# Kernel optimization log

Hardware: AMD Instinct MI355X
Metric: run time of the kernel (lower is better)

The kernel has to match this reference:

```python
import jax, jax.numpy as jnp
import numpy as np

OBS_LEN = 8
B = 262144
H = 16   # lstm hidden / MADE hidden / cond dim
D = 2    # trajectory input dim / flow dim
N_FLOWS = 4
CLAMP = 5.0


def _masks():
    # MADE masks for num_inputs=2, num_hidden=16 (ikostrikov get_mask)
    in_deg = jnp.arange(D) % D                      # [0, 1]
    hid_deg = jnp.zeros((H,), jnp.float32)          # arange(16) % (2-1) == 0
    out_deg = (jnp.arange(2 * D) % D - 1).astype(jnp.float32)  # [-1,0,-1,0]
    input_mask = (hid_deg[:, None] >= in_deg[None, :].astype(jnp.float32)).astype(jnp.float32)  # [16,2]
    hidden_mask = jnp.ones((H, H), jnp.float32)     # all degrees 0 -> full
    output_mask = (out_deg[:, None] >= hid_deg[None, :]).astype(jnp.float32)  # [4,16]
    return input_mask, hidden_mask, output_mask


def _made_ma(x, cond, p, masks):
    # x: [B,2], cond: [B,16] -> m, a: [B,2]
    im, hm, om = masks
    jW, jb, cW, hW, hb, oW, ob = p
    h = x @ (jW * im).T + jb + cond @ cW.T      # joiner (masked) + cond linear (no bias)
    h = jax.nn.relu(h)
    h = jax.nn.relu(h @ (hW * hm).T + hb)       # trunk hidden masked linear
    out = h @ (oW * om).T + ob                  # trunk output masked linear -> [B,4]
    m, a = out[:, :D], out[:, D:]
    a = CLAMP * jnp.tanh(a / CLAMP)             # soft log-scale clamp (clamp_flow)
    return m, a


def _made_inverse(u, cond, p, masks):
    x = jnp.zeros_like(u)
    for i in range(D):
        m, a = _made_ma(x, cond, p, masks)
        x = x.at[:, i].set(u[:, i] * jnp.exp(a[:, i]) + m[:, i])
    return x


def _maf_sample(noise, cond, made_params, masks):
    # modules = [MADE0,Rev,MADE1,Rev,MADE2,Rev,MADE3,Rev]; sample runs inverse in reversed order
    x = noise
    for k in reversed(range(N_FLOWS)):
        x = x[:, ::-1]                           # Reverse(2) inverse == flip
        p = tuple(t[k] for t in made_params)
        x = _made_inverse(x, cond, p, masks)
    return x


def _encode(traj, enc_W, enc_b, W_ih, W_hh, b_ih, b_hh, h0, c0):
    # obs_len LSTM loop; dropout is identity in eval/test mode
    def step(carry, x_t):
        h, c = carry
        e = jax.nn.relu(x_t @ enc_W.T + enc_b)                 # [B,16]
        g = e @ W_ih.T + b_ih + h @ W_hh.T + b_hh              # [B,64]
        i, f, gg, o = jnp.split(g, 4, axis=-1)                 # torch LSTMCell gate order
        c = jax.nn.sigmoid(f) * c + jax.nn.sigmoid(i) * jnp.tanh(gg)
        h = jax.nn.sigmoid(o) * jnp.tanh(c)
        return (h, c), None
    (h, c), _ = jax.lax.scan(step, (h0, c0), traj)
    return h


def setup_inputs() -> dict:
    key = jax.random.key(0)
    ks = jax.random.split(key, 16)
    s = 0.1
    return {
        "traj_rel": jax.random.normal(ks[0], (OBS_LEN + 1, B, D), jnp.float32),
        "obs_traj_pos": jax.random.normal(ks[1], (OBS_LEN, B, D), jnp.float32),
        "h0": jax.random.normal(ks[2], (B, H), jnp.float32),
        "c0": jax.random.normal(ks[3], (B, H), jnp.float32),
        "noise": jax.random.normal(ks[4], (B, D), jnp.float32),
        "enc_W": jax.random.normal(ks[5], (H, D), jnp.float32) * 0.2,
        "enc_b": jnp.zeros((H,), jnp.float32),
        "lstm_W_ih": jax.random.normal(ks[6], (4 * H, H), jnp.float32) * s,
        "lstm_W_hh": jax.random.normal(ks[7], (4 * H, H), jnp.float32) * 0.001,
        "lstm_b_ih": jnp.zeros((4 * H,), jnp.float32).at[H:2 * H].set(1.0),
        "lstm_b_hh": jnp.zeros((4 * H,), jnp.float32),
        "made_joiner_W": jax.random.normal(ks[8], (N_FLOWS, H, D), jnp.float32) * s,
        "made_joiner_b": jnp.zeros((N_FLOWS, H), jnp.float32),
        "made_cond_W": jax.random.normal(ks[9], (N_FLOWS, H, H), jnp.float32) * s,
        "made_hid_W": jax.random.normal(ks[10], (N_FLOWS, H, H), jnp.float32) * s,
        "made_hid_b": jnp.zeros((N_FLOWS, H), jnp.float32),
        "made_out_W": jax.random.normal(ks[11], (N_FLOWS, 2 * D, H), jnp.float32) * s,
        "made_out_b": jnp.zeros((N_FLOWS, 2 * D), jnp.float32),
    }


def reference(traj_rel, obs_traj_pos, h0, c0, noise,
              enc_W, enc_b, lstm_W_ih, lstm_W_hh, lstm_b_ih, lstm_b_hh,
              made_joiner_W, made_joiner_b, made_cond_W,
              made_hid_W, made_hid_b, made_out_W, made_out_b):
    masks = _masks()
    h = _encode(traj_rel[:OBS_LEN], enc_W, enc_b,
                lstm_W_ih, lstm_W_hh, lstm_b_ih, lstm_b_hh, h0, c0)  # [B,16]
    made_params = (made_joiner_W, made_joiner_b, made_cond_W,
                   made_hid_W, made_hid_b, made_out_W, made_out_b)
    goal = _maf_sample(noise, h, made_params, masks)                  # [B,2]
    return goal + obs_traj_pos[-1]                                    # mode='test' output_pred
```

## Files before the change

### kernel.cpp

```cpp
#include <hip/hip_runtime.h>

#define B_N 262144
#define OBS_N 8

typedef __attribute__((ext_vector_type(4))) _Float16 f16x4;
typedef __attribute__((ext_vector_type(2))) __fp16 fp16x2;
typedef __attribute__((ext_vector_type(4))) float f32x4;

#define LOG2E 1.44269504088896340736f

__device__ __forceinline__ float rcpf_(float x){ return __builtin_amdgcn_rcpf(x); }
__device__ __forceinline__ float exp2f_(float x){ return __builtin_amdgcn_exp2f(x); }
__device__ __forceinline__ float tanh_(float x){ return fmaf(-2.0f, rcpf_(exp2f_((2.0f*LOG2E) * x) + 1.0f), 1.0f); }

__device__ __forceinline__ f16x4 pack4(float a, float b, float c, float d){
    fp16x2 lo = __builtin_amdgcn_cvt_pkrtz(a, b);
    fp16x2 hi = __builtin_amdgcn_cvt_pkrtz(c, d);
    f16x4 r;
    r[0] = (_Float16)lo[0]; r[1] = (_Float16)lo[1];
    r[2] = (_Float16)hi[0]; r[3] = (_Float16)hi[1];
    return r;
}

#define MFMA16(a, b, c) __builtin_amdgcn_mfma_f32_16x16x16f16((a), (b), (c), 0, 0, 0)

__global__ __launch_bounds__(256, 4) void goal_kernel(
    const float* __restrict__ traj,
    const float* __restrict__ obsp,
    const float* __restrict__ h0,
    const float* __restrict__ c0,
    const float* __restrict__ noise,
    const float* __restrict__ encW,
    const float* __restrict__ encb,
    const float* __restrict__ Wih,
    const float* __restrict__ Whh,
    const float* __restrict__ bih,
    const float* __restrict__ bhh,
    const float* __restrict__ jW,
    const float* __restrict__ jb,
    const float* __restrict__ cW,
    const float* __restrict__ hW,
    const float* __restrict__ hb,
    const float* __restrict__ oW,
    const float* __restrict__ ob,
    float* __restrict__ out)
{
    const int lane = threadIdx.x & 63;
    const int wv   = threadIdx.x >> 6;
    const int q    = lane >> 4;
    const int s    = lane & 15;
    const int j4   = q * 4;
    const int base = blockIdx.x * 128 + wv * 32;
    const int colA = base + s;
    const int colB = base + 16 + s;

    f16x4 ew0h, ew1h, ebh;
    #pragma unroll
    for (int r = 0; r < 4; ++r) {
        ew0h[r] = (_Float16)encW[(j4 + r) * 2 + 0];
        ew1h[r] = (_Float16)encW[(j4 + r) * 2 + 1];
        ebh[r]  = (_Float16)encb[j4 + r];
    }

    const float gsc[4] = { -LOG2E, -LOG2E, -2.0f*LOG2E, -LOG2E };

    f16x4 wihA[4], whhA[4], biasH[4];
    #pragma unroll
    for (int m = 0; m < 4; ++m) {
        float4 wa = *(const float4*)(Wih + (16 * m + s) * 16 + j4);
        float4 wb = *(const float4*)(Whh + (16 * m + s) * 16 + j4);
        wihA[m] = pack4(wa.x*gsc[m], wa.y*gsc[m], wa.z*gsc[m], wa.w*gsc[m]);
        whhA[m] = pack4(wb.x*gsc[m], wb.y*gsc[m], wb.z*gsc[m], wb.w*gsc[m]);
        float4 b1 = *(const float4*)(bih + 16 * m + j4);
        float4 b2 = *(const float4*)(bhh + 16 * m + j4);
        biasH[m] = pack4((b1.x+b2.x)*gsc[m], (b1.y+b2.y)*gsc[m],
                         (b1.z+b2.z)*gsc[m], (b1.w+b2.w)*gsc[m]);
    }

    f32x4 cA = *(const f32x4*)(c0 + colA * 16 + j4);
    f32x4 cB = *(const f32x4*)(c0 + colB * 16 + j4);
    float4 hA0 = *(const float4*)(h0 + colA * 16 + j4);
    float4 hB0 = *(const float4*)(h0 + colB * 16 + j4);
    f16x4 hA = pack4(hA0.x, hA0.y, hA0.z, hA0.w);
    f16x4 hB = pack4(hB0.x, hB0.y, hB0.z, hB0.w);

    float2 nzA = *(const float2*)(noise + colA * 2);
    float2 nzB = *(const float2*)(noise + colB * 2);

    const float NEG2L2E = -2.0f * LOG2E;

    float2 xA = *(const float2*)(traj + colA * 2);
    float2 xB = *(const float2*)(traj + colB * 2);

    #pragma unroll 1
    for (int t = 0; t < OBS_N; ++t) {
        float2 nxA, nxB;
        if (t < OBS_N - 1) {
            nxA = *(const float2*)(traj + (t + 1) * (B_N * 2) + colA * 2);
            nxB = *(const float2*)(traj + (t + 1) * (B_N * 2) + colB * 2);
        }

        _Float16 ax = (_Float16)xA.x, ay = (_Float16)xA.y;
        _Float16 bx = (_Float16)xB.x, by = (_Float16)xB.y;
        f16x4 xxA = { ax, ax, ax, ax }, yyA = { ay, ay, ay, ay };
        f16x4 xxB = { bx, bx, bx, bx }, yyB = { by, by, by, by };
        f16x4 eA = ew0h * xxA + ew1h * yyA + ebh;
        f16x4 eB = ew0h * xxB + ew1h * yyB + ebh;
        #pragma unroll
        for (int r = 0; r < 4; ++r) {
            eA[r] = eA[r] > (_Float16)0 ? eA[r] : (_Float16)0;
            eB[r] = eB[r] > (_Float16)0 ? eB[r] : (_Float16)0;
        }

        f32x4 gA[4], gB[4];
        #pragma unroll
        for (int m = 0; m < 4; ++m) {
            f32x4 bv;
            bv[0] = (float)biasH[m][0]; bv[1] = (float)biasH[m][1];
            bv[2] = (float)biasH[m][2]; bv[3] = (float)biasH[m][3];
            gA[m] = MFMA16(wihA[m], eA, bv);
            gA[m] = MFMA16(whhA[m], hA, gA[m]);
            gB[m] = MFMA16(wihA[m], eB, bv);
            gB[m] = MFMA16(whhA[m], hB, gB[m]);
        }

        float hnA[4], hnB[4];
        #pragma unroll
        for (int r = 0; r < 4; ++r) {
            {
                float Ei = exp2f_(gA[0][r]);
                float Ef = exp2f_(gA[1][r]);
                float Eg = exp2f_(gA[2][r]);
                float Eo = exp2f_(gA[3][r]);
                float pi = 1.0f + Ei, pg = 1.0f + Eg, pf = 1.0f + Ef;
                float m_ = pi * pg;
                float R1 = rcpf_(m_ * pf);
                float cn = fmaf(cA[r], m_, fmaf(-Eg, pf, pf)) * R1;
                cA[r] = cn;
                float Ec = exp2f_(NEG2L2E * cn);
                float R2 = rcpf_((1.0f + Ec) * (1.0f + Eo));
                hnA[r] = fmaf(-Ec, R2, R2);
            }
            {
                float Ei = exp2f_(gB[0][r]);
                float Ef = exp2f_(gB[1][r]);
                float Eg = exp2f_(gB[2][r]);
                float Eo = exp2f_(gB[3][r]);
                float pi = 1.0f + Ei, pg = 1.0f + Eg, pf = 1.0f + Ef;
                float m_ = pi * pg;
                float R1 = rcpf_(m_ * pf);
                float cn = fmaf(cB[r], m_, fmaf(-Eg, pf, pf)) * R1;
                cB[r] = cn;
                float Ec = exp2f_(NEG2L2E * cn);
                float R2 = rcpf_((1.0f + Ec) * (1.0f + Eo));
                hnB[r] = fmaf(-Ec, R2, R2);
            }
        }
        hA = pack4(hnA[0], hnA[1], hnA[2], hnA[3]);
        hB = pack4(hnB[0], hnB[1], hnB[2], hnB[3]);

        if (t < OBS_N - 1) { xA = nxA; xB = nxB; }
    }

    float x0A = nzA.x, x1A = nzA.y;
    float x0B = nzB.x, x1B = nzB.y;

    #pragma unroll 1
    for (int kf = 3; kf >= 0; --kf) {
        float tA = x0A; x0A = x1A; x1A = tA;
        float tB = x0B; x0B = x1B; x1B = tB;

        float ob0 = ob[kf*4 + 0], ob1 = ob[kf*4 + 1];
        float ob2 = ob[kf*4 + 2], ob3 = ob[kf*4 + 3] * 0.2f;
        float ea0 = exp2f_(7.2134752044f * tanh_(ob2 * 0.2f));
        x0A = fmaf(x0A, ea0, ob0);
        x0B = fmaf(x0B, ea0, ob0);

        float4 cw = *(const float4*)(cW + kf * 256 + s * 16 + j4);
        f16x4 cwA = pack4(cw.x, cw.y, cw.z, cw.w);
        float4 hw = *(const float4*)(hW + kf * 256 + s * 16 + j4);
        f16x4 hwA = pack4(hw.x, hw.y, hw.z, hw.w);
        float osc = ((s & 3) == 3) ? 0.2f : 1.0f;
        float4 ow = *(const float4*)(oW + kf * 64 + (s & 3) * 16 + j4);
        f16x4 owA = pack4(ow.x * osc, ow.y * osc, ow.z * osc, ow.w * osc);

        f32x4 a1A, a1B;
        #pragma unroll
        for (int r = 0; r < 4; ++r) {
            float jwv = jW[kf * 32 + (j4 + r) * 2];
            float jbv = jb[kf * 16 + j4 + r];
            a1A[r] = fmaf(jwv, x0A, jbv);
            a1B[r] = fmaf(jwv, x0B, jbv);
        }
        a1A = MFMA16(cwA, hA, a1A);
        a1B = MFMA16(cwA, hB, a1B);
        f16x4 h1A = pack4(fmaxf(a1A[0],0.f), fmaxf(a1A[1],0.f), fmaxf(a1A[2],0.f), fmaxf(a1A[3],0.f));
        f16x4 h1B = pack4(fmaxf(a1B[0],0.f), fmaxf(a1B[1],0.f), fmaxf(a1B[2],0.f), fmaxf(a1B[3],0.f));

        f32x4 a2A, a2B;
        #pragma unroll
        for (int r = 0; r < 4; ++r) { float hbv = hb[kf * 16 + j4 + r]; a2A[r] = hbv; a2B[r] = hbv; }
        a2A = MFMA16(hwA, h1A, a2A);
        a2B = MFMA16(hwA, h1B, a2B);
        f16x4 h2A = pack4(fmaxf(a2A[0],0.f), fmaxf(a2A[1],0.f), fmaxf(a2A[2],0.f), fmaxf(a2A[3],0.f));
        f16x4 h2B = pack4(fmaxf(a2B[0],0.f), fmaxf(a2B[1],0.f), fmaxf(a2B[2],0.f), fmaxf(a2B[3],0.f));

        f32x4 a3A, a3B;
        a3A[0] = ob0; a3A[1] = ob1; a3A[2] = ob2; a3A[3] = ob3;
        a3B = a3A;
        a3A = MFMA16(owA, h2A, a3A);
        a3B = MFMA16(owA, h2B, a3B);

        x1A = fmaf(x1A, exp2f_(7.2134752044f * tanh_(a3A[3])), a3A[1]);
        x1B = fmaf(x1B, exp2f_(7.2134752044f * tanh_(a3B[3])), a3B[1]);
    }

    if (q == 0) {
        float2 ppA = *(const float2*)(obsp + (OBS_N - 1) * (B_N * 2) + colA * 2);
        float2 ppB = *(const float2*)(obsp + (OBS_N - 1) * (B_N * 2) + colB * 2);
        float2 oA; oA.x = x0A + ppA.x; oA.y = x1A + ppA.y;
        float2 oB; oB.x = x0B + ppB.x; oB.y = x1B + ppB.y;
        *(float2*)(out + colA * 2) = oA;
        *(float2*)(out + colB * 2) = oB;
    }
}

extern "C" void kernel_launch(void* const* d_in, const int* in_sizes, int n_in,
                              void* d_out, int out_size, void* d_ws, size_t ws_size,
                              hipStream_t stream) {
    goal_kernel<<<B_N / 128, 256, 0, stream>>>(
        (const float*)d_in[0],  (const float*)d_in[1],  (const float*)d_in[2],
        (const float*)d_in[3],  (const float*)d_in[4],  (const float*)d_in[5],
        (const float*)d_in[6],  (const float*)d_in[7],  (const float*)d_in[8],
        (const float*)d_in[9],  (const float*)d_in[10], (const float*)d_in[11],
        (const float*)d_in[12], (const float*)d_in[13], (const float*)d_in[14],
        (const float*)d_in[15], (const float*)d_in[16], (const float*)d_in[17],
        (float*)d_out);
}
```

Before: 44.32 us.

## Process LSTM column groups sequentially and raise occupancy target to five waves

```diff
diff --git a/kernel.cpp b/kernel.cpp
--- a/kernel.cpp
+++ b/kernel.cpp
@@ -24,7 +24,7 @@
 
 #define MFMA16(a, b, c) __builtin_amdgcn_mfma_f32_16x16x16f16((a), (b), (c), 0, 0, 0)
 
-__global__ __launch_bounds__(256, 4) void goal_kernel(
+__global__ __launch_bounds__(256, 5) void goal_kernel(
     const float* __restrict__ traj,
     const float* __restrict__ obsp,
     const float* __restrict__ h0,
@@ -112,26 +112,23 @@
             eB[r] = eB[r] > (_Float16)0 ? eB[r] : (_Float16)0;
         }
 
-        f32x4 gA[4], gB[4];
-        #pragma unroll
-        for (int m = 0; m < 4; ++m) {
-            f32x4 bv;
-            bv[0] = (float)biasH[m][0]; bv[1] = (float)biasH[m][1];
-            bv[2] = (float)biasH[m][2]; bv[3] = (float)biasH[m][3];
-            gA[m] = MFMA16(wihA[m], eA, bv);
-            gA[m] = MFMA16(whhA[m], hA, gA[m]);
-            gB[m] = MFMA16(wihA[m], eB, bv);
-            gB[m] = MFMA16(whhA[m], hB, gB[m]);
-        }
-
-        float hnA[4], hnB[4];
-        #pragma unroll
-        for (int r = 0; r < 4; ++r) {
-            {
-                float Ei = exp2f_(gA[0][r]);
-                float Ef = exp2f_(gA[1][r]);
-                float Eg = exp2f_(gA[2][r]);
-                float Eo = exp2f_(gA[3][r]);
+        {
+            f32x4 g[4];
+            #pragma unroll
+            for (int m = 0; m < 4; ++m) {
+                f32x4 bv;
+                bv[0] = (float)biasH[m][0]; bv[1] = (float)biasH[m][1];
+                bv[2] = (float)biasH[m][2]; bv[3] = (float)biasH[m][3];
+                g[m] = MFMA16(wihA[m], eA, bv);
+                g[m] = MFMA16(whhA[m], hA, g[m]);
+            }
+            float hn[4];
+            #pragma unroll
+            for (int r = 0; r < 4; ++r) {
+                float Ei = exp2f_(g[0][r]);
+                float Ef = exp2f_(g[1][r]);
+                float Eg = exp2f_(g[2][r]);
+                float Eo = exp2f_(g[3][r]);
                 float pi = 1.0f + Ei, pg = 1.0f + Eg, pf = 1.0f + Ef;
                 float m_ = pi * pg;
                 float R1 = rcpf_(m_ * pf);
@@ -139,13 +136,27 @@
                 cA[r] = cn;
                 float Ec = exp2f_(NEG2L2E * cn);
                 float R2 = rcpf_((1.0f + Ec) * (1.0f + Eo));
-                hnA[r] = fmaf(-Ec, R2, R2);
-            }
-            {
-                float Ei = exp2f_(gB[0][r]);
-                float Ef = exp2f_(gB[1][r]);
-                float Eg = exp2f_(gB[2][r]);
-                float Eo = exp2f_(gB[3][r]);
+                hn[r] = fmaf(-Ec, R2, R2);
+            }
+            hA = pack4(hn[0], hn[1], hn[2], hn[3]);
+        }
+        {
+            f32x4 g[4];
+            #pragma unroll
+            for (int m = 0; m < 4; ++m) {
+                f32x4 bv;
+                bv[0] = (float)biasH[m][0]; bv[1] = (float)biasH[m][1];
+                bv[2] = (float)biasH[m][2]; bv[3] = (float)biasH[m][3];
+                g[m] = MFMA16(wihA[m], eB, bv);
+                g[m] = MFMA16(whhA[m], hB, g[m]);
+            }
+            float hn[4];
+            #pragma unroll
+            for (int r = 0; r < 4; ++r) {
+                float Ei = exp2f_(g[0][r]);
+                float Ef = exp2f_(g[1][r]);
+                float Eg = exp2f_(g[2][r]);
+                float Eo = exp2f_(g[3][r]);
                 float pi = 1.0f + Ei, pg = 1.0f + Eg, pf = 1.0f + Ef;
                 float m_ = pi * pg;
                 float R1 = rcpf_(m_ * pf);
@@ -153,11 +164,10 @@
                 cB[r] = cn;
                 float Ec = exp2f_(NEG2L2E * cn);
                 float R2 = rcpf_((1.0f + Ec) * (1.0f + Eo));
-                hnB[r] = fmaf(-Ec, R2, R2);
-            }
-        }
-        hA = pack4(hnA[0], hnA[1], hnA[2], hnA[3]);
-        hB = pack4(hnB[0], hnB[1], hnB[2], hnB[3]);
+                hn[r] = fmaf(-Ec, R2, R2);
+            }
+            hB = pack4(hn[0], hn[1], hn[2], hn[3]);
+        }
 
         if (t < OBS_N - 1) { xA = nxA; xB = nxB; }
     }
```

After: 44.68 us. No clear change (+0.8%).

## Skew LSTM loop so one stream's MFMAs overlap the other's gate math

Applied to the files above, without the earlier changes.

```diff
diff --git a/kernel.cpp b/kernel.cpp
--- a/kernel.cpp
+++ b/kernel.cpp
@@ -89,30 +89,16 @@
 
     const float NEG2L2E = -2.0f * LOG2E;
 
-    float2 xA = *(const float2*)(traj + colA * 2);
     float2 xB = *(const float2*)(traj + colB * 2);
 
-    #pragma unroll 1
-    for (int t = 0; t < OBS_N; ++t) {
-        float2 nxA, nxB;
-        if (t < OBS_N - 1) {
-            nxA = *(const float2*)(traj + (t + 1) * (B_N * 2) + colA * 2);
-            nxB = *(const float2*)(traj + (t + 1) * (B_N * 2) + colB * 2);
-        }
-
-        _Float16 ax = (_Float16)xA.x, ay = (_Float16)xA.y;
-        _Float16 bx = (_Float16)xB.x, by = (_Float16)xB.y;
-        f16x4 xxA = { ax, ax, ax, ax }, yyA = { ay, ay, ay, ay };
-        f16x4 xxB = { bx, bx, bx, bx }, yyB = { by, by, by, by };
-        f16x4 eA = ew0h * xxA + ew1h * yyA + ebh;
-        f16x4 eB = ew0h * xxB + ew1h * yyB + ebh;
-        #pragma unroll
-        for (int r = 0; r < 4; ++r) {
-            eA[r] = eA[r] > (_Float16)0 ? eA[r] : (_Float16)0;
-            eB[r] = eB[r] > (_Float16)0 ? eB[r] : (_Float16)0;
-        }
-
-        f32x4 gA[4], gB[4];
+    f32x4 gA[4], gB[4];
+    {
+        float2 xA0 = *(const float2*)(traj + colA * 2);
+        _Float16 ax = (_Float16)xA0.x, ay = (_Float16)xA0.y;
+        f16x4 xx = { ax, ax, ax, ax }, yy = { ay, ay, ay, ay };
+        f16x4 eA = ew0h * xx + ew1h * yy + ebh;
+        #pragma unroll
+        for (int r = 0; r < 4; ++r) eA[r] = eA[r] > (_Float16)0 ? eA[r] : (_Float16)0;
         #pragma unroll
         for (int m = 0; m < 4; ++m) {
             f32x4 bv;
@@ -120,14 +106,34 @@
             bv[2] = (float)biasH[m][2]; bv[3] = (float)biasH[m][3];
             gA[m] = MFMA16(wihA[m], eA, bv);
             gA[m] = MFMA16(whhA[m], hA, gA[m]);
-            gB[m] = MFMA16(wihA[m], eB, bv);
-            gB[m] = MFMA16(whhA[m], hB, gB[m]);
-        }
-
-        float hnA[4], hnB[4];
-        #pragma unroll
-        for (int r = 0; r < 4; ++r) {
-            {
+        }
+    }
+
+    #pragma unroll 1
+    for (int t = 0; t < OBS_N; ++t) {
+        {
+            _Float16 bx = (_Float16)xB.x, by = (_Float16)xB.y;
+            f16x4 xx = { bx, bx, bx, bx }, yy = { by, by, by, by };
+            f16x4 eB = ew0h * xx + ew1h * yy + ebh;
+            #pragma unroll
+            for (int r = 0; r < 4; ++r) eB[r] = eB[r] > (_Float16)0 ? eB[r] : (_Float16)0;
+            #pragma unroll
+            for (int m = 0; m < 4; ++m) {
+                f32x4 bv;
+                bv[0] = (float)biasH[m][0]; bv[1] = (float)biasH[m][1];
+                bv[2] = (float)biasH[m][2]; bv[3] = (float)biasH[m][3];
+                gB[m] = MFMA16(wihA[m], eB, bv);
+                gB[m] = MFMA16(whhA[m], hB, gB[m]);
+            }
+        }
+
+        float2 nxA = *(const float2*)(traj + (t + 1) * (B_N * 2) + colA * 2);
+        float2 nxB = *(const float2*)(traj + (t + 1) * (B_N * 2) + colB * 2);
+
+        {
+            float hn[4];
+            #pragma unroll
+            for (int r = 0; r < 4; ++r) {
                 float Ei = exp2f_(gA[0][r]);
                 float Ef = exp2f_(gA[1][r]);
                 float Eg = exp2f_(gA[2][r]);
@@ -139,9 +145,31 @@
                 cA[r] = cn;
                 float Ec = exp2f_(NEG2L2E * cn);
                 float R2 = rcpf_((1.0f + Ec) * (1.0f + Eo));
-                hnA[r] = fmaf(-Ec, R2, R2);
-            }
-            {
+                hn[r] = fmaf(-Ec, R2, R2);
+            }
+            hA = pack4(hn[0], hn[1], hn[2], hn[3]);
+        }
+
+        {
+            _Float16 ax = (_Float16)nxA.x, ay = (_Float16)nxA.y;
+            f16x4 xx = { ax, ax, ax, ax }, yy = { ay, ay, ay, ay };
+            f16x4 eA = ew0h * xx + ew1h * yy + ebh;
+            #pragma unroll
+            for (int r = 0; r < 4; ++r) eA[r] = eA[r] > (_Float16)0 ? eA[r] : (_Float16)0;
+            #pragma unroll
+            for (int m = 0; m < 4; ++m) {
+                f32x4 bv;
+                bv[0] = (float)biasH[m][0]; bv[1] = (float)biasH[m][1];
+                bv[2] = (float)biasH[m][2]; bv[3] = (float)biasH[m][3];
+                gA[m] = MFMA16(wihA[m], eA, bv);
+                gA[m] = MFMA16(whhA[m], hA, gA[m]);
+            }
+        }
+
+        {
+            float hn[4];
+            #pragma unroll
+            for (int r = 0; r < 4; ++r) {
                 float Ei = exp2f_(gB[0][r]);
                 float Ef = exp2f_(gB[1][r]);
                 float Eg = exp2f_(gB[2][r]);
@@ -153,13 +181,12 @@
                 cB[r] = cn;
                 float Ec = exp2f_(NEG2L2E * cn);
                 float R2 = rcpf_((1.0f + Ec) * (1.0f + Eo));
-                hnB[r] = fmaf(-Ec, R2, R2);
-            }
-        }
-        hA = pack4(hnA[0], hnA[1], hnA[2], hnA[3]);
-        hB = pack4(hnB[0], hnB[1], hnB[2], hnB[3]);
-
-        if (t < OBS_N - 1) { xA = nxA; xB = nxB; }
+                hn[r] = fmaf(-Ec, R2, R2);
+            }
+            hB = pack4(hn[0], hn[1], hn[2], hn[3]);
+        }
+
+        xB = nxB;
     }
 
     float x0A = nzA.x, x1A = nzA.y;
```

Measured after the change: 46.77 us. 1.06x slower.
